# Kernel optimization log

Measured on AMD Instinct MI355X. Metric: run time of the kernel, lower is better.

Reference implementation:

```python
import jax, jax.numpy as jnp
import numpy as np

CH = 128
GROUPS = 8
HEADS = 8
HEAD_DIM = CH // HEADS  # 16
EPS = 1e-5


def setup_inputs() -> dict:
    key = jax.random.key(0)
    ks = jax.random.split(key, 5)
    x = jax.random.normal(ks[0], (8, CH, 128, 128), dtype=jnp.float32)
    gn_w = jnp.ones((CH,), dtype=jnp.float32)
    gn_b = jnp.zeros((CH,), dtype=jnp.float32)
    w_in = jax.random.normal(ks[1], (CH, CH), dtype=jnp.float32) * (1.0 / np.sqrt(CH))
    b_in = jax.random.normal(ks[2], (CH,), dtype=jnp.float32) * 0.01
    w_out = jax.random.normal(ks[3], (CH, CH), dtype=jnp.float32) * (1.0 / np.sqrt(CH))
    b_out = jax.random.normal(ks[4], (CH,), dtype=jnp.float32) * 0.01
    return {"x": x, "gn_w": gn_w, "gn_b": gn_b, "w_in": w_in, "b_in": b_in,
            "w_out": w_out, "b_out": b_out}


def _group_norm(x, gamma, beta):
    b, c, H, W = x.shape
    xg = x.reshape(b, GROUPS, c // GROUPS, H, W)
    mean = xg.mean(axis=(2, 3, 4), keepdims=True)
    var = xg.var(axis=(2, 3, 4), keepdims=True)
    xg = (xg - mean) * jax.lax.rsqrt(var + EPS)
    x = xg.reshape(b, c, H, W)
    return x * gamma[None, :, None, None] + beta[None, :, None, None]


def _conv1x1(x, w, bias):
    # w: [out_c, in_c] (1x1 conv == pointwise matmul over channels)
    return jnp.einsum('oc,bchw->bohw', w, x) + bias[None, :, None, None]


def reference(x, gn_w, gn_b, w_in, b_in, w_out, b_out):
    b, c, H, W = x.shape
    h = _group_norm(x, gn_w, gn_b)
    h = _conv1x1(h, w_in, b_in)
    # reshape to [b, heads, head_dim, H*W]; attention over head_dim axis,
    # contracting the spatial axis (d = H*W) as in the original einsums
    hh = h.reshape(b, HEADS, HEAD_DIM, H * W)
    scale = HEAD_DIM ** (-0.5)
    scores = jnp.einsum('bhid,bhjd->bhij', hh, hh) * scale  # [b,heads,hd,hd]
    weights = jax.nn.softmax(scores, axis=-1)
    attn = jnp.einsum('bhij,bhjd->bhid', weights, hh)
    attn = attn.reshape(b, c, H, W)
    h = _conv1x1(attn, w_out, b_out)
    return x + h
```

## Files before the change

### kernel.cpp

```cpp
#include <hip/hip_runtime.h>


#define NPOS 16384
#define PITCH 136

typedef short short8 __attribute__((ext_vector_type(8)));
typedef float f32x4 __attribute__((ext_vector_type(4)));

__device__ __forceinline__ unsigned short f2bf(float f) {
    union { float f; unsigned u; } v; v.f = f;
    unsigned r = (v.u + 0x7fffu + ((v.u >> 16) & 1u)) >> 16;
    return (unsigned short)r;
}

__global__ __launch_bounds__(256) void k_stats(const float* __restrict__ x,
                                               float* __restrict__ stats) {
    const float4* p = (const float4*)(x + (size_t)blockIdx.x * 16384);
    int t = threadIdx.x;
    float s1 = 0.f, s2 = 0.f;
#pragma unroll
    for (int j = 0; j < 16; ++j) {
        float4 v = p[t + j * 256];
        s1 += v.x + v.y + v.z + v.w;
        s2 += v.x * v.x + v.y * v.y + v.z * v.z + v.w * v.w;
    }
    for (int off = 32; off; off >>= 1) {
        s1 += __shfl_down(s1, off);
        s2 += __shfl_down(s2, off);
    }
    __shared__ float r1[4], r2[4];
    int wv = t >> 6;
    if ((t & 63) == 0) { r1[wv] = s1; r2[wv] = s2; }
    __syncthreads();
    if (t == 0) {
        s1 = r1[0] + r1[1] + r1[2] + r1[3];
        s2 = r2[0] + r2[1] + r2[2] + r2[3];
        int bg = blockIdx.x >> 4;
        atomicAdd(&stats[bg * 2 + 0], s1);
        atomicAdd(&stats[bg * 2 + 1], s2);
    }
}

__global__ __launch_bounds__(128) void k_prep(const float* __restrict__ stats,
                                              const float* __restrict__ gn_w,
                                              const float* __restrict__ gn_b,
                                              const float* __restrict__ w_in,
                                              const float* __restrict__ b_in,
                                              float* __restrict__ sA,
                                              float* __restrict__ vA) {
    int b = blockIdx.x, c = threadIdx.x;
    int g = c >> 4;
    float s1 = stats[(b * 8 + g) * 2 + 0];
    float s2 = stats[(b * 8 + g) * 2 + 1];
    const float invN = 1.0f / 262144.0f;
    float mean = s1 * invN;
    float var = s2 * invN - mean * mean;
    float rstd = rsqrtf(var + 1e-5f);
    float s = gn_w[c] * rstd;
    float tt = gn_b[c] - mean * s;
    __shared__ float tl[128];
    tl[c] = tt;
    sA[b * 128 + c] = s;
    __syncthreads();
    float v = b_in[c];
    const float* wr = w_in + c * 128;
#pragma unroll 8
    for (int k = 0; k < 128; ++k) v += wr[k] * tl[k];
    vA[b * 128 + c] = v;
}

__global__ __launch_bounds__(256, 2) void k_gemm1_scores(const float* __restrict__ x,
                                                         const float* __restrict__ w_in,
                                                         const float* __restrict__ sA,
                                                         const float* __restrict__ vA,
                                                         float* __restrict__ Sg) {
    __shared__ unsigned short As[128 * PITCH];
    __shared__ unsigned short Xt[128 * PITCH];
    __shared__ float v_s[128];

    const int t = threadIdx.x;
    const int lane = t & 63, wv = t >> 6;
    const int q = lane >> 4, i16 = lane & 15;
    const int b = blockIdx.x >> 7;
    const int p0 = (blockIdx.x & 127) << 7;

    if (t < 128) v_s[t] = vA[b * 128 + t];

    {
        const float4* w4 = (const float4*)w_in;
        const float4* s4 = (const float4*)(sA + b * 128);
#pragma unroll
        for (int i = 0; i < 16; ++i) {
            int idx = t + i * 256;
            int c = idx >> 5, k4 = idx & 31;
            float4 w = w4[idx];
            float4 s = s4[k4];
            ushort4 o;
            o.x = f2bf(w.x * s.x); o.y = f2bf(w.y * s.y);
            o.z = f2bf(w.z * s.z); o.w = f2bf(w.w * s.w);
            *(ushort4*)&As[c * PITCH + k4 * 4] = o;
        }
    }
    {
        const float* xb = x + (size_t)b * (128 * NPOS) + p0;
#pragma unroll
        for (int i = 0; i < 16; ++i) {
            int p = ((i & 1) << 6) + lane;
            int kq = (wv << 3) + (i >> 1);
            const float* col = xb + (size_t)(kq * 4) * NPOS + p;
            float a0 = col[0];
            float a1 = col[NPOS];
            float a2 = col[2 * NPOS];
            float a3 = col[3 * NPOS];
            ushort4 o; o.x = f2bf(a0); o.y = f2bf(a1); o.z = f2bf(a2); o.w = f2bf(a3);
            *(ushort4*)&Xt[p * PITCH + kq * 4] = o;
        }
    }
    __syncthreads();

    f32x4 acc[2][8];
#pragma unroll
    for (int a = 0; a < 2; ++a)
#pragma unroll
        for (int pt = 0; pt < 8; ++pt) acc[a][pt] = (f32x4){0.f, 0.f, 0.f, 0.f};

#pragma unroll
    for (int ks = 0; ks < 4; ++ks) {
        short8 a0 = *(const short8*)&As[(wv * 32 + i16) * PITCH + ks * 32 + q * 8];
        short8 a1 = *(const short8*)&As[(wv * 32 + 16 + i16) * PITCH + ks * 32 + q * 8];
#pragma unroll
        for (int pt = 0; pt < 8; ++pt) {
            short8 bb = *(const short8*)&Xt[(pt * 16 + i16) * PITCH + ks * 32 + q * 8];
            acc[0][pt] = __builtin_amdgcn_mfma_f32_16x16x32_bf16(a0, bb, acc[0][pt], 0, 0, 0);
            acc[1][pt] = __builtin_amdgcn_mfma_f32_16x16x32_bf16(a1, bb, acc[1][pt], 0, 0, 0);
        }
    }
    __syncthreads();

    unsigned short* Hs = Xt;
#pragma unroll
    for (int a = 0; a < 2; ++a) {
        int cbase = wv * 32 + a * 16 + q * 4;
#pragma unroll
        for (int pt = 0; pt < 8; ++pt) {
            int p = pt * 16 + i16;
#pragma unroll
            for (int r = 0; r < 4; ++r) {
                int c = cbase + r;
                Hs[c * PITCH + p] = f2bf(acc[a][pt][r] + v_s[c]);
            }
        }
    }
    __syncthreads();

#pragma unroll
    for (int hh = 0; hh < 2; ++hh) {
        int h = wv * 2 + hh;
        f32x4 sacc = (f32x4){0.f, 0.f, 0.f, 0.f};
#pragma unroll
        for (int ks = 0; ks < 4; ++ks) {
            short8 f = *(const short8*)&Hs[(h * 16 + i16) * PITCH + ks * 32 + q * 8];
            sacc = __builtin_amdgcn_mfma_f32_16x16x32_bf16(f, f, sacc, 0, 0, 0);
        }
        float* sg = Sg + (b * 8 + h) * 256;
#pragma unroll
        for (int r = 0; r < 4; ++r)
            atomicAdd(&sg[(q * 4 + r) * 16 + i16], sacc[r]);
    }
}

__global__ __launch_bounds__(256) void k_softmax_weff(const float* __restrict__ Sg,
                                                      const float* __restrict__ w_out,
                                                      float* __restrict__ weff) {
    int b = blockIdx.x, t = threadIdx.x;
    __shared__ float W[2048];
    if (t < 128) {
        const float* row = Sg + b * 2048 + t * 16;
        float v[16];
        float m = -1e30f;
#pragma unroll
        for (int j = 0; j < 16; ++j) { v[j] = row[j] * 0.25f; m = fmaxf(m, v[j]); }
        float sum = 0.f;
#pragma unroll
        for (int j = 0; j < 16; ++j) { v[j] = __expf(v[j] - m); sum += v[j]; }
        float inv = 1.0f / sum;
#pragma unroll
        for (int j = 0; j < 16; ++j) W[t * 16 + j] = v[j] * inv;
    }
    __syncthreads();
    float* wo = weff + b * 16384;
#pragma unroll 2
    for (int n = 0; n < 64; ++n) {
        int idx = t + n * 256;
        int c = idx >> 7, k = idx & 127;
        int h = k >> 4, j = k & 15;
        const float* wr = w_out + c * 128 + h * 16;
        const float* Wr = W + h * 256 + j;
        float a = 0.f;
#pragma unroll
        for (int i = 0; i < 16; ++i) a += wr[i] * Wr[i * 16];
        wo[idx] = a;
    }
}

__global__ __launch_bounds__(256, 2) void k_attn_out(const float* __restrict__ x,
                                                     const float* __restrict__ w_in,
                                                     const float* __restrict__ sA,
                                                     const float* __restrict__ vA,
                                                     const float* __restrict__ weff,
                                                     const float* __restrict__ b_out,
                                                     float* __restrict__ out) {
    __shared__ unsigned short As[128 * PITCH];
    __shared__ unsigned short Xt[128 * PITCH];
    __shared__ float v_s[128];
    __shared__ float bo_s[128];

    const int t = threadIdx.x;
    const int lane = t & 63, wv = t >> 6;
    const int q = lane >> 4, i16 = lane & 15;
    const int b = blockIdx.x >> 7;
    const int p0 = (blockIdx.x & 127) << 7;

    if (t < 128) { v_s[t] = vA[b * 128 + t]; bo_s[t] = b_out[t]; }

    const float* xb = x + (size_t)b * (128 * NPOS) + p0;

    {
        const float4* w4 = (const float4*)w_in;
        const float4* s4 = (const float4*)(sA + b * 128);
#pragma unroll
        for (int i = 0; i < 16; ++i) {
            int idx = t + i * 256;
            int c = idx >> 5, k4 = idx & 31;
            float4 w = w4[idx];
            float4 s = s4[k4];
            ushort4 o;
            o.x = f2bf(w.x * s.x); o.y = f2bf(w.y * s.y);
            o.z = f2bf(w.z * s.z); o.w = f2bf(w.w * s.w);
            *(ushort4*)&As[c * PITCH + k4 * 4] = o;
        }
    }
    {
#pragma unroll
        for (int i = 0; i < 16; ++i) {
            int p = ((i & 1) << 6) + lane;
            int kq = (wv << 3) + (i >> 1);
            const float* col = xb + (size_t)(kq * 4) * NPOS + p;
            float a0 = col[0];
            float a1 = col[NPOS];
            float a2 = col[2 * NPOS];
            float a3 = col[3 * NPOS];
            ushort4 o; o.x = f2bf(a0); o.y = f2bf(a1); o.z = f2bf(a2); o.w = f2bf(a3);
            *(ushort4*)&Xt[p * PITCH + kq * 4] = o;
        }
    }
    __syncthreads();

    f32x4 acc[2][8];
#pragma unroll
    for (int a = 0; a < 2; ++a)
#pragma unroll
        for (int pt = 0; pt < 8; ++pt) acc[a][pt] = (f32x4){0.f, 0.f, 0.f, 0.f};

#pragma unroll
    for (int ks = 0; ks < 4; ++ks) {
        short8 a0 = *(const short8*)&As[(wv * 32 + i16) * PITCH + ks * 32 + q * 8];
        short8 a1 = *(const short8*)&As[(wv * 32 + 16 + i16) * PITCH + ks * 32 + q * 8];
#pragma unroll
        for (int pt = 0; pt < 8; ++pt) {
            short8 bb = *(const short8*)&Xt[(pt * 16 + i16) * PITCH + ks * 32 + q * 8];
            acc[0][pt] = __builtin_amdgcn_mfma_f32_16x16x32_bf16(a0, bb, acc[0][pt], 0, 0, 0);
            acc[1][pt] = __builtin_amdgcn_mfma_f32_16x16x32_bf16(a1, bb, acc[1][pt], 0, 0, 0);
        }
    }
    __syncthreads();

#pragma unroll
    for (int a = 0; a < 2; ++a) {
        int cb = wv * 32 + a * 16 + q * 4;
#pragma unroll
        for (int pt = 0; pt < 8; ++pt) {
            int p = pt * 16 + i16;
            ushort4 o;
            o.x = f2bf(acc[a][pt][0] + v_s[cb + 0]);
            o.y = f2bf(acc[a][pt][1] + v_s[cb + 1]);
            o.z = f2bf(acc[a][pt][2] + v_s[cb + 2]);
            o.w = f2bf(acc[a][pt][3] + v_s[cb + 3]);
            *(ushort4*)&Xt[p * PITCH + cb] = o;
        }
    }
    {
        const float4* w4 = (const float4*)(weff + b * 16384);
#pragma unroll
        for (int i = 0; i < 16; ++i) {
            int idx = t + i * 256;
            int c = idx >> 5, k4 = idx & 31;
            float4 w = w4[idx];
            ushort4 o;
            o.x = f2bf(w.x); o.y = f2bf(w.y); o.z = f2bf(w.z); o.w = f2bf(w.w);
            *(ushort4*)&As[c * PITCH + k4 * 4] = o;
        }
    }
    __syncthreads();

#pragma unroll
    for (int a = 0; a < 2; ++a)
#pragma unroll
        for (int pt = 0; pt < 8; ++pt) acc[a][pt] = (f32x4){0.f, 0.f, 0.f, 0.f};

#pragma unroll
    for (int ks = 0; ks < 4; ++ks) {
        short8 a0 = *(const short8*)&As[(wv * 32 + i16) * PITCH + ks * 32 + q * 8];
        short8 a1 = *(const short8*)&As[(wv * 32 + 16 + i16) * PITCH + ks * 32 + q * 8];
#pragma unroll
        for (int pt = 0; pt < 8; ++pt) {
            short8 bb = *(const short8*)&Xt[(pt * 16 + i16) * PITCH + ks * 32 + q * 8];
            acc[0][pt] = __builtin_amdgcn_mfma_f32_16x16x32_bf16(a0, bb, acc[0][pt], 0, 0, 0);
            acc[1][pt] = __builtin_amdgcn_mfma_f32_16x16x32_bf16(a1, bb, acc[1][pt], 0, 0, 0);
        }
    }

    float* ob = out + (size_t)b * (128 * NPOS) + p0;
#pragma unroll
    for (int a = 0; a < 2; ++a) {
        int cb = wv * 32 + a * 16 + q * 4;
#pragma unroll
        for (int pt = 0; pt < 8; ++pt) {
            int p = pt * 16 + i16;
#pragma unroll
            for (int r = 0; r < 4; ++r) {
                int c = cb + r;
                ob[(size_t)c * NPOS + p] = acc[a][pt][r] + bo_s[c] + xb[(size_t)c * NPOS + p];
            }
        }
    }
}

extern "C" void kernel_launch(void* const* d_in, const int* in_sizes, int n_in,
                              void* d_out, int out_size, void* d_ws, size_t ws_size,
                              hipStream_t stream) {
    const float* x    = (const float*)d_in[0];
    const float* gn_w = (const float*)d_in[1];
    const float* gn_b = (const float*)d_in[2];
    const float* w_in = (const float*)d_in[3];
    const float* b_in = (const float*)d_in[4];
    const float* w_out= (const float*)d_in[5];
    const float* b_out= (const float*)d_in[6];
    float* out = (float*)d_out;

    float* ws    = (float*)d_ws;
    float* stats = ws;
    float* Sg    = ws + 128;
    float* sA    = ws + 16512;
    float* vA    = ws + 17536;
    float* weff  = ws + 18560;

    hipMemsetAsync(d_ws, 0, (128 + 16384) * sizeof(float), stream);
    k_stats<<<dim3(1024), dim3(256), 0, stream>>>(x, stats);
    k_prep<<<dim3(8), dim3(128), 0, stream>>>(stats, gn_w, gn_b, w_in, b_in, sA, vA);
    k_gemm1_scores<<<dim3(1024), dim3(256), 0, stream>>>(x, w_in, sA, vA, Sg);
    k_softmax_weff<<<dim3(8), dim3(256), 0, stream>>>(Sg, w_out, weff);
    k_attn_out<<<dim3(1024), dim3(256), 0, stream>>>(x, w_in, sA, vA, weff, b_out, out);
}
```

Baseline: 195.7 us.

## Materialize bf16 projected activations and precompute bf16 weights to skip recomputing GEMM1

GEMM1 now writes the projected activations h as bf16 to a workspace buffer (position-major tiles). The output kernel reads that buffer instead of reloading x and redoing the first projection. The scaled input weights and the effective output weights are converted to bf16 once in the small prep and softmax kernels, and MFMA A operands are read straight from global memory rather than staged in LDS. LDS use drops, so the occupancy hint goes from 2 to 4 blocks per CU. The epilogue stages results in LDS for coalesced float4 residual reads and writes. The cost is an extra 32 MB bf16 write plus read of h, and the output now goes through bf16 rounding before the residual add.

Result: slower. 214.9 us (+9.8%).

```diff
diff --git a/kernel.cpp b/kernel.cpp
--- a/kernel.cpp
+++ b/kernel.cpp
@@ -11,6 +11,10 @@
     union { float f; unsigned u; } v; v.f = f;
     unsigned r = (v.u + 0x7fffu + ((v.u >> 16) & 1u)) >> 16;
     return (unsigned short)r;
+}
+__device__ __forceinline__ float bf2f(unsigned short h) {
+    union { unsigned u; float f; } v; v.u = ((unsigned)h) << 16;
+    return v.f;
 }
 
 __global__ __launch_bounds__(256) void k_stats(const float* __restrict__ x,
@@ -41,40 +45,56 @@
     }
 }
 
-__global__ __launch_bounds__(128) void k_prep(const float* __restrict__ stats,
+__global__ __launch_bounds__(256) void k_prep(const float* __restrict__ stats,
                                               const float* __restrict__ gn_w,
                                               const float* __restrict__ gn_b,
                                               const float* __restrict__ w_in,
                                               const float* __restrict__ b_in,
-                                              float* __restrict__ sA,
-                                              float* __restrict__ vA) {
-    int b = blockIdx.x, c = threadIdx.x;
-    int g = c >> 4;
-    float s1 = stats[(b * 8 + g) * 2 + 0];
-    float s2 = stats[(b * 8 + g) * 2 + 1];
-    const float invN = 1.0f / 262144.0f;
-    float mean = s1 * invN;
-    float var = s2 * invN - mean * mean;
-    float rstd = rsqrtf(var + 1e-5f);
-    float s = gn_w[c] * rstd;
-    float tt = gn_b[c] - mean * s;
-    __shared__ float tl[128];
-    tl[c] = tt;
-    sA[b * 128 + c] = s;
-    __syncthreads();
-    float v = b_in[c];
-    const float* wr = w_in + c * 128;
+                                              float* __restrict__ vA,
+                                              unsigned short* __restrict__ Asb) {
+    int b = blockIdx.x, t = threadIdx.x;
+    __shared__ float ss[128], tl[128];
+    if (t < 128) {
+        int g = t >> 4;
+        float s1 = stats[(b * 8 + g) * 2 + 0];
+        float s2 = stats[(b * 8 + g) * 2 + 1];
+        const float invN = 1.0f / 262144.0f;
+        float mean = s1 * invN;
+        float var = s2 * invN - mean * mean;
+        float rstd = rsqrtf(var + 1e-5f);
+        float s = gn_w[t] * rstd;
+        ss[t] = s;
+        tl[t] = gn_b[t] - mean * s;
+    }
+    __syncthreads();
+    if (t < 128) {
+        float v = b_in[t];
+        const float* wr = w_in + t * 128;
 #pragma unroll 8
-    for (int k = 0; k < 128; ++k) v += wr[k] * tl[k];
-    vA[b * 128 + c] = v;
-}
-
-__global__ __launch_bounds__(256, 2) void k_gemm1_scores(const float* __restrict__ x,
-                                                         const float* __restrict__ w_in,
-                                                         const float* __restrict__ sA,
+        for (int k = 0; k < 128; ++k) v += wr[k] * tl[k];
+        vA[b * 128 + t] = v;
+    }
+    unsigned short* ab = Asb + b * 16384;
+    const float4* w4 = (const float4*)w_in;
+#pragma unroll
+    for (int i = 0; i < 16; ++i) {
+        int idx = t + i * 256;
+        int c = idx >> 5, k4 = idx & 31;
+        float4 w = w4[idx];
+        ushort4 o;
+        o.x = f2bf(w.x * ss[k4 * 4 + 0]);
+        o.y = f2bf(w.y * ss[k4 * 4 + 1]);
+        o.z = f2bf(w.z * ss[k4 * 4 + 2]);
+        o.w = f2bf(w.w * ss[k4 * 4 + 3]);
+        *(ushort4*)&ab[c * 128 + k4 * 4] = o;
+    }
+}
+
+__global__ __launch_bounds__(256, 4) void k_gemm1_scores(const float* __restrict__ x,
+                                                         const unsigned short* __restrict__ Asb,
                                                          const float* __restrict__ vA,
+                                                         unsigned short* __restrict__ h1t,
                                                          float* __restrict__ Sg) {
-    __shared__ unsigned short As[128 * PITCH];
     __shared__ unsigned short Xt[128 * PITCH];
     __shared__ float v_s[128];
 
@@ -82,25 +102,11 @@
     const int lane = t & 63, wv = t >> 6;
     const int q = lane >> 4, i16 = lane & 15;
     const int b = blockIdx.x >> 7;
-    const int p0 = (blockIdx.x & 127) << 7;
+    const int tile = blockIdx.x & 127;
+    const int p0 = tile << 7;
 
     if (t < 128) v_s[t] = vA[b * 128 + t];
 
-    {
-        const float4* w4 = (const float4*)w_in;
-        const float4* s4 = (const float4*)(sA + b * 128);
-#pragma unroll
-        for (int i = 0; i < 16; ++i) {
-            int idx = t + i * 256;
-            int c = idx >> 5, k4 = idx & 31;
-            float4 w = w4[idx];
-            float4 s = s4[k4];
-            ushort4 o;
-            o.x = f2bf(w.x * s.x); o.y = f2bf(w.y * s.y);
-            o.z = f2bf(w.z * s.z); o.w = f2bf(w.w * s.w);
-            *(ushort4*)&As[c * PITCH + k4 * 4] = o;
-        }
-    }
     {
         const float* xb = x + (size_t)b * (128 * NPOS) + p0;
 #pragma unroll
@@ -118,6 +124,8 @@
     }
     __syncthreads();
 
+    const unsigned short* ab = Asb + b * 16384;
+
     f32x4 acc[2][8];
 #pragma unroll
     for (int a = 0; a < 2; ++a)
@@ -126,8 +134,8 @@
 
 #pragma unroll
     for (int ks = 0; ks < 4; ++ks) {
-        short8 a0 = *(const short8*)&As[(wv * 32 + i16) * PITCH + ks * 32 + q * 8];
-        short8 a1 = *(const short8*)&As[(wv * 32 + 16 + i16) * PITCH + ks * 32 + q * 8];
+        short8 a0 = *(const short8*)&ab[(wv * 32 + i16) * 128 + ks * 32 + q * 8];
+        short8 a1 = *(const short8*)&ab[(wv * 32 + 16 + i16) * 128 + ks * 32 + q * 8];
 #pragma unroll
         for (int pt = 0; pt < 8; ++pt) {
             short8 bb = *(const short8*)&Xt[(pt * 16 + i16) * PITCH + ks * 32 + q * 8];
@@ -138,17 +146,23 @@
     __syncthreads();
 
     unsigned short* Hs = Xt;
+    unsigned short* h1tb = h1t + (size_t)(b * 128 + tile) * 16384;
 #pragma unroll
     for (int a = 0; a < 2; ++a) {
-        int cbase = wv * 32 + a * 16 + q * 4;
+        int cb = wv * 32 + a * 16 + q * 4;
 #pragma unroll
         for (int pt = 0; pt < 8; ++pt) {
             int p = pt * 16 + i16;
-#pragma unroll
-            for (int r = 0; r < 4; ++r) {
-                int c = cbase + r;
-                Hs[c * PITCH + p] = f2bf(acc[a][pt][r] + v_s[c]);
-            }
+            ushort4 o;
+            o.x = f2bf(acc[a][pt][0] + v_s[cb + 0]);
+            o.y = f2bf(acc[a][pt][1] + v_s[cb + 1]);
+            o.z = f2bf(acc[a][pt][2] + v_s[cb + 2]);
+            o.w = f2bf(acc[a][pt][3] + v_s[cb + 3]);
+            Hs[(cb + 0) * PITCH + p] = o.x;
+            Hs[(cb + 1) * PITCH + p] = o.y;
+            Hs[(cb + 2) * PITCH + p] = o.z;
+            Hs[(cb + 3) * PITCH + p] = o.w;
+            *(ushort4*)&h1tb[p * 128 + cb] = o;
         }
     }
     __syncthreads();
@@ -171,7 +185,7 @@
 
 __global__ __launch_bounds__(256) void k_softmax_weff(const float* __restrict__ Sg,
                                                       const float* __restrict__ w_out,
-                                                      float* __restrict__ weff) {
+                                                      unsigned short* __restrict__ weffb) {
     int b = blockIdx.x, t = threadIdx.x;
     __shared__ float W[2048];
     if (t < 128) {
@@ -188,7 +202,7 @@
         for (int j = 0; j < 16; ++j) W[t * 16 + j] = v[j] * inv;
     }
     __syncthreads();
-    float* wo = weff + b * 16384;
+    unsigned short* wo = weffb + b * 16384;
 #pragma unroll 2
     for (int n = 0; n < 64; ++n) {
         int idx = t + n * 256;
@@ -199,62 +213,29 @@
         float a = 0.f;
 #pragma unroll
         for (int i = 0; i < 16; ++i) a += wr[i] * Wr[i * 16];
-        wo[idx] = a;
-    }
-}
-
-__global__ __launch_bounds__(256, 2) void k_attn_out(const float* __restrict__ x,
-                                                     const float* __restrict__ w_in,
-                                                     const float* __restrict__ sA,
-                                                     const float* __restrict__ vA,
-                                                     const float* __restrict__ weff,
+        wo[idx] = f2bf(a);
+    }
+}
+
+__global__ __launch_bounds__(256, 4) void k_attn_out(const float* __restrict__ x,
+                                                     const unsigned short* __restrict__ weffb,
+                                                     const unsigned short* __restrict__ h1t,
                                                      const float* __restrict__ b_out,
                                                      float* __restrict__ out) {
-    __shared__ unsigned short As[128 * PITCH];
-    __shared__ unsigned short Xt[128 * PITCH];
-    __shared__ float v_s[128];
+    __shared__ unsigned short Hb[128 * PITCH];
     __shared__ float bo_s[128];
 
     const int t = threadIdx.x;
     const int lane = t & 63, wv = t >> 6;
     const int q = lane >> 4, i16 = lane & 15;
     const int b = blockIdx.x >> 7;
-    const int p0 = (blockIdx.x & 127) << 7;
-
-    if (t < 128) { v_s[t] = vA[b * 128 + t]; bo_s[t] = b_out[t]; }
-
-    const float* xb = x + (size_t)b * (128 * NPOS) + p0;
-
-    {
-        const float4* w4 = (const float4*)w_in;
-        const float4* s4 = (const float4*)(sA + b * 128);
-#pragma unroll
-        for (int i = 0; i < 16; ++i) {
-            int idx = t + i * 256;
-            int c = idx >> 5, k4 = idx & 31;
-            float4 w = w4[idx];
-            float4 s = s4[k4];
-            ushort4 o;
-            o.x = f2bf(w.x * s.x); o.y = f2bf(w.y * s.y);
-            o.z = f2bf(w.z * s.z); o.w = f2bf(w.w * s.w);
-            *(ushort4*)&As[c * PITCH + k4 * 4] = o;
-        }
-    }
-    {
-#pragma unroll
-        for (int i = 0; i < 16; ++i) {
-            int p = ((i & 1) << 6) + lane;
-            int kq = (wv << 3) + (i >> 1);
-            const float* col = xb + (size_t)(kq * 4) * NPOS + p;
-            float a0 = col[0];
-            float a1 = col[NPOS];
-            float a2 = col[2 * NPOS];
-            float a3 = col[3 * NPOS];
-            ushort4 o; o.x = f2bf(a0); o.y = f2bf(a1); o.z = f2bf(a2); o.w = f2bf(a3);
-            *(ushort4*)&Xt[p * PITCH + kq * 4] = o;
-        }
-    }
-    __syncthreads();
+    const int tile = blockIdx.x & 127;
+    const int p0 = tile << 7;
+
+    if (t < 128) bo_s[t] = b_out[t];
+
+    const unsigned short* ab = weffb + b * 16384;
+    const unsigned short* h1tb = h1t + (size_t)(b * 128 + tile) * 16384;
 
     f32x4 acc[2][8];
 #pragma unroll
@@ -264,11 +245,11 @@
 
 #pragma unroll
     for (int ks = 0; ks < 4; ++ks) {
-        short8 a0 = *(const short8*)&As[(wv * 32 + i16) * PITCH + ks * 32 + q * 8];
-        short8 a1 = *(const short8*)&As[(wv * 32 + 16 + i16) * PITCH + ks * 32 + q * 8];
+        short8 a0 = *(const short8*)&ab[(wv * 32 + i16) * 128 + ks * 32 + q * 8];
+        short8 a1 = *(const short8*)&ab[(wv * 32 + 16 + i16) * 128 + ks * 32 + q * 8];
 #pragma unroll
         for (int pt = 0; pt < 8; ++pt) {
-            short8 bb = *(const short8*)&Xt[(pt * 16 + i16) * PITCH + ks * 32 + q * 8];
+            short8 bb = *(const short8*)&h1tb[(pt * 16 + i16) * 128 + ks * 32 + q * 8];
             acc[0][pt] = __builtin_amdgcn_mfma_f32_16x16x32_bf16(a0, bb, acc[0][pt], 0, 0, 0);
             acc[1][pt] = __builtin_amdgcn_mfma_f32_16x16x32_bf16(a1, bb, acc[1][pt], 0, 0, 0);
         }
@@ -281,58 +262,28 @@
 #pragma unroll
         for (int pt = 0; pt < 8; ++pt) {
             int p = pt * 16 + i16;
-            ushort4 o;
-            o.x = f2bf(acc[a][pt][0] + v_s[cb + 0]);
-            o.y = f2bf(acc[a][pt][1] + v_s[cb + 1]);
-            o.z = f2bf(acc[a][pt][2] + v_s[cb + 2]);
-            o.w = f2bf(acc[a][pt][3] + v_s[cb + 3]);
-            *(ushort4*)&Xt[p * PITCH + cb] = o;
-        }
-    }
-    {
-        const float4* w4 = (const float4*)(weff + b * 16384);
-#pragma unroll
-        for (int i = 0; i < 16; ++i) {
-            int idx = t + i * 256;
-            int c = idx >> 5, k4 = idx & 31;
-            float4 w = w4[idx];
-            ushort4 o;
-            o.x = f2bf(w.x); o.y = f2bf(w.y); o.z = f2bf(w.z); o.w = f2bf(w.w);
-            *(ushort4*)&As[c * PITCH + k4 * 4] = o;
-        }
-    }
-    __syncthreads();
-
-#pragma unroll
-    for (int a = 0; a < 2; ++a)
-#pragma unroll
-        for (int pt = 0; pt < 8; ++pt) acc[a][pt] = (f32x4){0.f, 0.f, 0.f, 0.f};
-
-#pragma unroll
-    for (int ks = 0; ks < 4; ++ks) {
-        short8 a0 = *(const short8*)&As[(wv * 32 + i16) * PITCH + ks * 32 + q * 8];
-        short8 a1 = *(const short8*)&As[(wv * 32 + 16 + i16) * PITCH + ks * 32 + q * 8];
-#pragma unroll
-        for (int pt = 0; pt < 8; ++pt) {
-            short8 bb = *(const short8*)&Xt[(pt * 16 + i16) * PITCH + ks * 32 + q * 8];
-            acc[0][pt] = __builtin_amdgcn_mfma_f32_16x16x32_bf16(a0, bb, acc[0][pt], 0, 0, 0);
-            acc[1][pt] = __builtin_amdgcn_mfma_f32_16x16x32_bf16(a1, bb, acc[1][pt], 0, 0, 0);
-        }
-    }
-
+            Hb[(cb + 0) * PITCH + p] = f2bf(acc[a][pt][0] + bo_s[cb + 0]);
+            Hb[(cb + 1) * PITCH + p] = f2bf(acc[a][pt][1] + bo_s[cb + 1]);
+            Hb[(cb + 2) * PITCH + p] = f2bf(acc[a][pt][2] + bo_s[cb + 2]);
+            Hb[(cb + 3) * PITCH + p] = f2bf(acc[a][pt][3] + bo_s[cb + 3]);
+        }
+    }
+    __syncthreads();
+
+    const float* xb = x + (size_t)b * (128 * NPOS) + p0;
     float* ob = out + (size_t)b * (128 * NPOS) + p0;
 #pragma unroll
-    for (int a = 0; a < 2; ++a) {
-        int cb = wv * 32 + a * 16 + q * 4;
-#pragma unroll
-        for (int pt = 0; pt < 8; ++pt) {
-            int p = pt * 16 + i16;
-#pragma unroll
-            for (int r = 0; r < 4; ++r) {
-                int c = cb + r;
-                ob[(size_t)c * NPOS + p] = acc[a][pt][r] + bo_s[c] + xb[(size_t)c * NPOS + p];
-            }
-        }
+    for (int i = 0; i < 16; ++i) {
+        int idx = t + i * 256;
+        int c = idx >> 5, p4 = idx & 31;
+        ushort4 hv = *(const ushort4*)&Hb[c * PITCH + p4 * 4];
+        const float4 xv = *(const float4*)&xb[(size_t)c * NPOS + p4 * 4];
+        float4 o;
+        o.x = xv.x + bf2f(hv.x);
+        o.y = xv.y + bf2f(hv.y);
+        o.z = xv.z + bf2f(hv.z);
+        o.w = xv.w + bf2f(hv.w);
+        *(float4*)&ob[(size_t)c * NPOS + p4 * 4] = o;
     }
 }
 
@@ -351,14 +302,15 @@
     float* ws    = (float*)d_ws;
     float* stats = ws;
     float* Sg    = ws + 128;
-    float* sA    = ws + 16512;
-    float* vA    = ws + 17536;
-    float* weff  = ws + 18560;
+    float* vA    = ws + 16512;
+    unsigned short* Asb   = (unsigned short*)(ws + 17536);
+    unsigned short* weffb = (unsigned short*)(ws + 83072);
+    unsigned short* h1t   = (unsigned short*)(ws + 148608);
 
     hipMemsetAsync(d_ws, 0, (128 + 16384) * sizeof(float), stream);
     k_stats<<<dim3(1024), dim3(256), 0, stream>>>(x, stats);
-    k_prep<<<dim3(8), dim3(128), 0, stream>>>(stats, gn_w, gn_b, w_in, b_in, sA, vA);
-    k_gemm1_scores<<<dim3(1024), dim3(256), 0, stream>>>(x, w_in, sA, vA, Sg);
-    k_softmax_weff<<<dim3(8), dim3(256), 0, stream>>>(Sg, w_out, weff);
-    k_attn_out<<<dim3(1024), dim3(256), 0, stream>>>(x, w_in, sA, vA, weff, b_out, out);
-}
+    k_prep<<<dim3(8), dim3(256), 0, stream>>>(stats, gn_w, gn_b, w_in, b_in, vA, Asb);
+    k_gemm1_scores<<<dim3(1024), dim3(256), 0, stream>>>(x, Asb, vA, h1t, Sg);
+    k_softmax_weff<<<dim3(8), dim3(256), 0, stream>>>(Sg, w_out, weffb);
+    k_attn_out<<<dim3(1024), dim3(256), 0, stream>>>(x, weffb, h1t, b_out, out);
+}
```
